# Kernel tuning notes

Hardware: AMD Instinct MI355X
Metric: run time of the kernel (lower is better)

The kernel has to match this reference:

```python
import jax, jax.numpy as jnp
import numpy as np
from jax import lax

N = 4096
IN_DIM, HID, OUT_DIM = 8, 64, 4
N_CONV = 10


def setup_inputs() -> dict:
    key = jax.random.key(0)
    ks = jax.random.split(key, 16)
    s = 0.05
    inp = {
        "inputs": jax.random.normal(ks[0], (N, IN_DIM), jnp.float32),
        "emb_w": jax.random.normal(ks[1], (IN_DIM, HID), jnp.float32) * s,
        "emb_b": jnp.zeros((HID,), jnp.float32),
        "q_w": jax.random.normal(ks[2], (HID, HID), jnp.float32) * s,
        "q_b": jnp.zeros((HID,), jnp.float32),
        "k_w": jax.random.normal(ks[3], (HID, HID), jnp.float32) * s,
        "k_b": jnp.zeros((HID,), jnp.float32),
        # 10 asymmetric conv layers: 1x3 kernel, 3x1 kernel, PReLU scalar (torch default 0.25)
        "conv_w1": jax.random.normal(ks[4], (N_CONV, 3), jnp.float32) * 0.3,
        "conv_w2": jax.random.normal(ks[5], (N_CONV, 3), jnp.float32) * 0.3,
        "conv_a": jnp.full((N_CONV,), 0.25, jnp.float32),
        "gcn_w": jax.random.normal(ks[6], (OUT_DIM, HID), jnp.float32) * s,
        "gcn_b": jnp.zeros((HID,), jnp.float32),
        "gcn_a": jnp.float32(0.25),
        "mlp_w1": jax.random.normal(ks[7], (HID, HID // 2), jnp.float32) * s,
        "mlp_b1": jnp.zeros((HID // 2,), jnp.float32),
        "mlp_w2": jax.random.normal(ks[8], (HID // 2, OUT_DIM), jnp.float32) * s,
        "mlp_b2": jnp.zeros((OUT_DIM,), jnp.float32),
    }
    return inp


def _asym_layer(x, w1, w2, a):
    # x: [1,1,N,N]; w1 -> 1x3 conv, w2 -> 3x1 conv, a -> PReLU scalar
    k1 = w1.reshape(1, 1, 1, 3)
    k2 = w2.reshape(1, 1, 3, 1)
    dn = ("NCHW", "OIHW", "NCHW")
    o = (lax.conv_general_dilated(x, k1, (1, 1), [(0, 0), (1, 1)], dimension_numbers=dn)
         + lax.conv_general_dilated(x, k2, (1, 1), [(1, 1), (0, 0)], dimension_numbers=dn))
    return jnp.where(o >= 0, o, a * o)


def reference(inputs, emb_w, emb_b, q_w, q_b, k_w, k_b,
              conv_w1, conv_w2, conv_a,
              gcn_w, gcn_b, gcn_a, mlp_w1, mlp_b1, mlp_w2, mlp_b2):
    o = inputs[:, 4:]                                   # [N, 4]
    x = inputs @ emb_w + emb_b                          # [N, H]
    q = x @ q_w + q_b                                   # [N, D]
    k = x @ k_w + k_b                                   # [N, D]
    scores = (q @ k.T) / jnp.sqrt(jnp.float32(k.shape[-1]))
    attn = jax.nn.softmax(scores, axis=-1)              # [N, N]

    h = attn[None, None]                                # [1,1,N,N]
    for i in range(N_CONV):
        h = _asym_layer(h, conv_w1[i], conv_w2[i], conv_a[i])
    conv_features = h[0, 0]                             # [N, N]

    mask = (jax.nn.sigmoid(conv_features) > 0.5).astype(attn.dtype)
    adjacency = mask * attn                             # [N, N]
    calc = adjacency @ o                                # [N, 4]

    g = calc @ gcn_w + gcn_b
    g = jnp.where(g >= 0, g, gcn_a * g)                 # PReLU
    m = jnp.maximum(g @ mlp_w1 + mlp_b1, 0.0)
    return m @ mlp_w2 + mlp_b2                          # [N, 4]
```

## Files before the change

kernel.cpp:

```cpp
#include <hip/hip_runtime.h>
#include <hip/hip_fp16.h>

#define NROWS 4096
#define HID 64

typedef _Float16 f16x8 __attribute__((ext_vector_type(8)));
typedef float f32x4 __attribute__((ext_vector_type(4)));

static __device__ __forceinline__ __half2 u2h(unsigned u) {
  __half2 h; __builtin_memcpy(&h, &u, 4); return h;
}
static __device__ __forceinline__ unsigned h2u(__half2 h) {
  unsigned u; __builtin_memcpy(&u, &h, 4); return u;
}

__global__ __launch_bounds__(256) void k_embed(
    const float* __restrict__ inp, const float* __restrict__ emb_w,
    const float* __restrict__ emb_b, const float* __restrict__ q_w,
    const float* __restrict__ q_b, const float* __restrict__ k_w,
    const float* __restrict__ k_b, __half* __restrict__ qh,
    __half* __restrict__ kh, float* __restrict__ opk) {
  int t = threadIdx.x;
  int rr = t >> 6;
  int c = t & 63;
  int row = blockIdx.x * 4 + rr;
  __shared__ float in_s[4][8];
  __shared__ float x_s[4][64];
  if (c < 8) in_s[rr][c] = inp[row * 8 + c];
  __syncthreads();
  float acc = emb_b[c];
#pragma unroll
  for (int i = 0; i < 8; ++i) acc += in_s[rr][i] * emb_w[i * 64 + c];
  x_s[rr][c] = acc;
  __syncthreads();
  float qa = q_b[c], ka = k_b[c];
#pragma unroll
  for (int i = 0; i < 64; ++i) {
    float xv = x_s[rr][i];
    qa += xv * q_w[i * 64 + c];
    ka += xv * k_w[i * 64 + c];
  }
  qh[row * 64 + c] = __float2half(qa * 0.125f);
  kh[row * 64 + c] = __float2half(ka);
  if (c < 4) opk[row * 4 + c] = inp[row * 8 + 4 + c];
}

__global__ __launch_bounds__(512, 2) void k_scores(
    const __half* __restrict__ qh, const __half* __restrict__ kh,
    float* __restrict__ S) {
  __shared__ float redm[8][16];
  __shared__ float reds[8][16];
  int t = threadIdx.x;
  int w = t >> 6;
  int l = t & 63;
  int m16 = l & 15;
  int g4 = l >> 4;
  int rb = blockIdx.x * 16;
  const uint4* qq = (const uint4*)qh;
  const uint4* kk = (const uint4*)kh;
  int qrow = rb + m16;
  f16x8 a0 = __builtin_bit_cast(f16x8, qq[qrow * 8 + g4]);
  f16x8 a1 = __builtin_bit_cast(f16x8, qq[qrow * 8 + 4 + g4]);
  f32x4 acc[32];
#pragma unroll
  for (int i = 0; i < 32; ++i) acc[i] = (f32x4){0.f, 0.f, 0.f, 0.f};
#pragma unroll
  for (int i = 0; i < 32; ++i) {
    int kcol = (w * 32 + i) * 16 + m16;
    f16x8 b0 = __builtin_bit_cast(f16x8, kk[kcol * 8 + g4]);
    f16x8 b1 = __builtin_bit_cast(f16x8, kk[kcol * 8 + 4 + g4]);
    acc[i] = __builtin_amdgcn_mfma_f32_16x16x32_f16(a0, b0, acc[i], 0, 0, 0);
    acc[i] = __builtin_amdgcn_mfma_f32_16x16x32_f16(a1, b1, acc[i], 0, 0, 0);
  }
  float m4[4] = {-1e30f, -1e30f, -1e30f, -1e30f};
#pragma unroll
  for (int i = 0; i < 32; ++i) {
#pragma unroll
    for (int c = 0; c < 4; ++c) m4[c] = fmaxf(m4[c], acc[i][c]);
  }
#pragma unroll
  for (int off = 1; off < 16; off <<= 1) {
#pragma unroll
    for (int c = 0; c < 4; ++c) m4[c] = fmaxf(m4[c], __shfl_xor(m4[c], off, 64));
  }
  if (m16 == 0) {
#pragma unroll
    for (int c = 0; c < 4; ++c) redm[w][g4 * 4 + c] = m4[c];
  }
  __syncthreads();
#pragma unroll
  for (int c = 0; c < 4; ++c) {
    float mm = redm[0][g4 * 4 + c];
#pragma unroll
    for (int ww = 1; ww < 8; ++ww) mm = fmaxf(mm, redm[ww][g4 * 4 + c]);
    m4[c] = mm;
  }
  float s4[4] = {0.f, 0.f, 0.f, 0.f};
#pragma unroll
  for (int i = 0; i < 32; ++i) {
#pragma unroll
    for (int c = 0; c < 4; ++c) {
      float e = __expf(acc[i][c] - m4[c]);
      acc[i][c] = e;
      s4[c] += e;
    }
  }
#pragma unroll
  for (int off = 1; off < 16; off <<= 1) {
#pragma unroll
    for (int c = 0; c < 4; ++c) s4[c] += __shfl_xor(s4[c], off, 64);
  }
  if (m16 == 0) {
#pragma unroll
    for (int c = 0; c < 4; ++c) reds[w][g4 * 4 + c] = s4[c];
  }
  __syncthreads();
  float li[4];
#pragma unroll
  for (int c = 0; c < 4; ++c) {
    float ss = reds[0][g4 * 4 + c];
#pragma unroll
    for (int ww = 1; ww < 8; ++ww) ss += reds[ww][g4 * 4 + c];
    li[c] = 1.0f / ss;
  }
#pragma unroll
  for (int i = 0; i < 32; ++i) {
    int col = (w * 32 + i) * 16 + m16;
#pragma unroll
    for (int c = 0; c < 4; ++c) {
      S[(size_t)(rb + g4 * 4 + c) * NROWS + col] = acc[i][c] * li[c];
    }
  }
}

#define C5D 130
#define C5H 74
#define C5OW 236
#define C5OH 54
#define C5GX 18
#define C5GY 76

__global__ __launch_bounds__(512, 2) void k_conv5(
    const float* __restrict__ attn, float* __restrict__ partial,
    const float* __restrict__ w1p, const float* __restrict__ w2p,
    const float* __restrict__ ap, const float* __restrict__ opk) {
  __shared__ unsigned buf[C5H * C5D];
  int tid = threadIdx.x;
  int bx = blockIdx.x, by = blockIdx.y;
  int gi0 = by * C5OH - 10;
  int gj0 = bx * C5OW - 10;
  bool edge = (bx == 0) || (bx == C5GX - 1) || (by == 0) || (by == C5GY - 1);
  if (!edge) {
    for (int idx = tid; idx < C5H * 128; idx += 512) {
      int r = idx >> 7, d = idx & 127;
      float2 v = *(const float2*)(attn + (size_t)(gi0 + r) * NROWS + gj0 + 2 * d);
      buf[r * C5D + d] =
          h2u(__float22half2_rn(make_float2(v.x * 256.f, v.y * 256.f)));
    }
  } else {
    for (int idx = tid; idx < C5H * 128; idx += 512) {
      int r = idx >> 7, d = idx & 127;
      int gi = gi0 + r, gj = gj0 + 2 * d;
      float a = 0.f, b = 0.f;
      if ((unsigned)gi < (unsigned)NROWS) {
        if ((unsigned)gj < (unsigned)NROWS) a = attn[(size_t)gi * NROWS + gj] * 256.f;
        if ((unsigned)(gj + 1) < (unsigned)NROWS) b = attn[(size_t)gi * NROWS + gj + 1] * 256.f;
      }
      buf[r * C5D + d] = h2u(__float22half2_rn(make_float2(a, b)));
    }
  }
  __syncthreads();

  int wv = tid >> 6, l = tid & 63;
  int rb = 1 + 9 * wv;
  int doff = 2 * l;
  __half2 CM0 = __float2half2_rn(1.f), CM1 = __float2half2_rn(1.f);
  if (edge) {
    float m0 = ((unsigned)(gj0 + 4 * l + 0) < (unsigned)NROWS) ? 1.f : 0.f;
    float m1 = ((unsigned)(gj0 + 4 * l + 1) < (unsigned)NROWS) ? 1.f : 0.f;
    float m2 = ((unsigned)(gj0 + 4 * l + 2) < (unsigned)NROWS) ? 1.f : 0.f;
    float m3 = ((unsigned)(gj0 + 4 * l + 3) < (unsigned)NROWS) ? 1.f : 0.f;
    CM0 = __float22half2_rn(make_float2(m0, m1));
    CM1 = __float22half2_rn(make_float2(m2, m3));
  }

  for (int p = 0; p < 10; ++p) {
    __half2 W10 = __float2half2_rn(w1p[3 * p]);
    __half2 W12 = __float2half2_rn(w1p[3 * p + 2]);
    __half2 WC  = __float2half2_rn(w1p[3 * p + 1] + w2p[3 * p + 1]);
    __half2 W20 = __float2half2_rn(w2p[3 * p]);
    __half2 W22 = __float2half2_rn(w2p[3 * p + 2]);
    __half2 AL  = __float2half2_rn(ap[p]);
    uint2 Vm = *(uint2*)&buf[(rb - 1) * C5D + doff];
    uint2 Vc = *(uint2*)&buf[rb * C5D + doff];
    uint2 dfirst, dlast;
#pragma unroll
    for (int s = 0; s < 9; ++s) {
      int r = rb + s;
      uint2 Vp = *(uint2*)&buf[(r + 1) * C5D + doff];
      unsigned Lm1 = (unsigned)__builtin_amdgcn_update_dpp(
          0, (int)Vc.y, 0x138, 0xF, 0xF, true);
      unsigned Hp1 = (unsigned)__builtin_amdgcn_update_dpp(
          0, (int)Vc.x, 0x130, 0xF, 0xF, true);
      unsigned SL0 = __builtin_amdgcn_alignbit(Vc.x, Lm1, 16);
      unsigned SR0 = __builtin_amdgcn_alignbit(Vc.y, Vc.x, 16);
      unsigned SR1 = __builtin_amdgcn_alignbit(Hp1, Vc.y, 16);
      __half2 o0 = __hmul2(WC, u2h(Vc.x));
      o0 = __hfma2(W10, u2h(SL0), o0);
      o0 = __hfma2(W12, u2h(SR0), o0);
      o0 = __hfma2(W20, u2h(Vm.x), o0);
      o0 = __hfma2(W22, u2h(Vp.x), o0);
      __half2 o1 = __hmul2(WC, u2h(Vc.y));
      o1 = __hfma2(W10, u2h(SR0), o1);
      o1 = __hfma2(W12, u2h(SR1), o1);
      o1 = __hfma2(W20, u2h(Vm.y), o1);
      o1 = __hfma2(W22, u2h(Vp.y), o1);
      {
        unsigned u0 = h2u(o0), ua0 = h2u(__hmul2(AL, o0)), r0;
        asm("v_pk_max_f16 %0, %1, %2" : "=v"(r0) : "v"(u0), "v"(ua0));
        o0 = u2h(r0);
        unsigned u1 = h2u(o1), ua1 = h2u(__hmul2(AL, o1)), r1;
        asm("v_pk_max_f16 %0, %1, %2" : "=v"(r1) : "v"(u1), "v"(ua1));
        o1 = u2h(r1);
      }
      if (edge) {
        o0 = __hmul2(o0, CM0);
        o1 = __hmul2(o1, CM1);
        if ((unsigned)(gi0 + r) >= (unsigned)NROWS) {
          o0 = __float2half2_rn(0.f);
          o1 = __float2half2_rn(0.f);
        }
      }
      uint2 res = {h2u(o0), h2u(o1)};
      if (s == 0) dfirst = res;
      else if (s == 8) dlast = res;
      else *(uint2*)&buf[r * C5D + doff] = res;
      Vm = Vc; Vc = Vp;
    }
    __syncthreads();
    *(uint2*)&buf[rb * C5D + doff] = dfirst;
    *(uint2*)&buf[(rb + 8) * C5D + doff] = dlast;
    __syncthreads();
  }

  const unsigned* fin = buf;
  int i = tid >> 3;
  int part = tid & 7;
  int gi = gi0 + 10 + i;
  float a0 = 0.f, a1 = 0.f, a2 = 0.f, a3 = 0.f;
  if (i < C5OH && gi < NROWS) {
    const float4* op = (const float4*)opk;
    for (int g = part; g < 59; g += 8) {
      int jc = 10 + 4 * g;
      int gj = gj0 + jc;
      if (gj + 3 < NROWS) {
        unsigned d0 = fin[(10 + i) * C5D + (jc >> 1)];
        unsigned d1 = fin[(10 + i) * C5D + (jc >> 1) + 1];
        __half2 h0 = u2h(d0), h1 = u2h(d1);
        float4 av = *(const float4*)(attn + (size_t)gi * NROWS + gj);
        if (__low2float(h0) > 0.f)  { float4 o = op[gj + 0]; a0 += av.x * o.x; a1 += av.x * o.y; a2 += av.x * o.z; a3 += av.x * o.w; }
        if (__high2float(h0) > 0.f) { float4 o = op[gj + 1]; a0 += av.y * o.x; a1 += av.y * o.y; a2 += av.y * o.z; a3 += av.y * o.w; }
        if (__low2float(h1) > 0.f)  { float4 o = op[gj + 2]; a0 += av.z * o.x; a1 += av.z * o.y; a2 += av.z * o.z; a3 += av.z * o.w; }
        if (__high2float(h1) > 0.f) { float4 o = op[gj + 3]; a0 += av.w * o.x; a1 += av.w * o.y; a2 += av.w * o.z; a3 += av.w * o.w; }
      }
    }
  }
#pragma unroll
  for (int off = 1; off < 8; off <<= 1) {
    a0 += __shfl_xor(a0, off, 64);
    a1 += __shfl_xor(a1, off, 64);
    a2 += __shfl_xor(a2, off, 64);
    a3 += __shfl_xor(a3, off, 64);
  }
  if (part == 0 && i < C5OH && gi < NROWS) {
    float4 r = {a0, a1, a2, a3};
    *(float4*)&partial[((size_t)bx * NROWS + gi) * 4] = r;
  }
}

__global__ __launch_bounds__(64) void k_head(
    const float* __restrict__ partial, const float* __restrict__ gcn_w,
    const float* __restrict__ gcn_b, const float* __restrict__ gcn_a,
    const float* __restrict__ w1, const float* __restrict__ b1,
    const float* __restrict__ w2, const float* __restrict__ b2,
    float* __restrict__ out) {
  int row = blockIdx.x;
  int t = threadIdx.x;
  __shared__ float c4[4];
  __shared__ float gs[64];
  __shared__ float ms[32];
  {
    int c = t & 3, gg = t >> 2;
    float s = partial[((size_t)gg * NROWS + row) * 4 + c];
    if (gg < C5GX - 16)
      s += partial[((size_t)(gg + 16) * NROWS + row) * 4 + c];
#pragma unroll
    for (int off = 4; off < 64; off <<= 1) s += __shfl_xor(s, off, 64);
    if (t < 4) c4[t] = s;
  }
  __syncthreads();
  float g = gcn_b[t];
#pragma unroll
  for (int d = 0; d < 4; ++d) g += c4[d] * gcn_w[d * 64 + t];
  float ga = gcn_a[0];
  gs[t] = (g >= 0.f) ? g : ga * g;
  __syncthreads();
  if (t < 32) {
    float mm = b1[t];
#pragma unroll
    for (int i = 0; i < 64; ++i) mm += gs[i] * w1[i * 32 + t];
    ms[t] = fmaxf(mm, 0.f);
  }
  __syncthreads();
  if (t < 4) {
    float o = b2[t];
#pragma unroll
    for (int i = 0; i < 32; ++i) o += ms[i] * w2[i * 4 + t];
    out[row * 4 + t] = o;
  }
}

extern "C" void kernel_launch(void* const* d_in, const int* in_sizes, int n_in,
                              void* d_out, int out_size, void* d_ws, size_t ws_size,
                              hipStream_t stream) {
  (void)in_sizes; (void)n_in; (void)out_size; (void)ws_size;
  const float* inp    = (const float*)d_in[0];
  const float* emb_w  = (const float*)d_in[1];
  const float* emb_b  = (const float*)d_in[2];
  const float* q_w    = (const float*)d_in[3];
  const float* q_b    = (const float*)d_in[4];
  const float* k_w    = (const float*)d_in[5];
  const float* k_b    = (const float*)d_in[6];
  const float* conv_w1 = (const float*)d_in[7];
  const float* conv_w2 = (const float*)d_in[8];
  const float* conv_a  = (const float*)d_in[9];
  const float* gcn_w  = (const float*)d_in[10];
  const float* gcn_b  = (const float*)d_in[11];
  const float* gcn_a  = (const float*)d_in[12];
  const float* mlp_w1 = (const float*)d_in[13];
  const float* mlp_b1 = (const float*)d_in[14];
  const float* mlp_w2 = (const float*)d_in[15];
  const float* mlp_b2 = (const float*)d_in[16];
  float* out = (float*)d_out;

  const size_t NN = (size_t)NROWS * NROWS;
  float* A       = (float*)d_ws;
  float* partial = A + NN;
  float* qhf     = partial + (size_t)18 * NROWS * 4;
  float* khf     = qhf + (size_t)NROWS * HID / 2;
  float* opk     = khf + (size_t)NROWS * HID / 2;

  k_embed<<<NROWS / 4, 256, 0, stream>>>(inp, emb_w, emb_b, q_w, q_b, k_w, k_b,
                                         (__half*)qhf, (__half*)khf, opk);
  k_scores<<<NROWS / 16, 512, 0, stream>>>((const __half*)qhf,
                                           (const __half*)khf, A);
  k_conv5<<<dim3(C5GX, C5GY), 512, 0, stream>>>(A, partial, conv_w1, conv_w2,
                                                conv_a, opk);
  k_head<<<NROWS, 64, 0, stream>>>(partial, gcn_w, gcn_b, gcn_a, mlp_w1, mlp_b1,
                                   mlp_w2, mlp_b2, out);
}
```

Baseline: 121.2 us.

## Store attention matrix in fp16 pre-scaled, resize conv tiles, batch head rows

The scores kernel now writes the softmax output as fp16 pre-multiplied by 256 instead of fp32, halving the N×N write and the conv kernel's read traffic. The conv kernel loads the half2 data straight into shared memory without conversion, and the final mask-times-attn accumulation reads fp16 attn and rescales by 1/256 at the end. Conv tile height drops from 54 to 46 output rows (8 rows per wave), which raises halo overhead but may improve occupancy via smaller shared memory. The head kernel processes 8 rows per 512-thread block instead of one row per 64-thread block. Using fp16 attn values in the adjacency product adds rounding error.

```diff
diff --git a/kernel.cpp b/kernel.cpp
--- a/kernel.cpp
+++ b/kernel.cpp
@@ -47,7 +47,7 @@
 
 __global__ __launch_bounds__(512, 2) void k_scores(
     const __half* __restrict__ qh, const __half* __restrict__ kh,
-    float* __restrict__ S) {
+    __half* __restrict__ Sh) {
   __shared__ float redm[8][16];
   __shared__ float reds[8][16];
   int t = threadIdx.x;
@@ -121,58 +121,59 @@
     float ss = reds[0][g4 * 4 + c];
 #pragma unroll
     for (int ww = 1; ww < 8; ++ww) ss += reds[ww][g4 * 4 + c];
-    li[c] = 1.0f / ss;
+    li[c] = 256.0f / ss;
   }
 #pragma unroll
   for (int i = 0; i < 32; ++i) {
     int col = (w * 32 + i) * 16 + m16;
 #pragma unroll
     for (int c = 0; c < 4; ++c) {
-      S[(size_t)(rb + g4 * 4 + c) * NROWS + col] = acc[i][c] * li[c];
+      Sh[(size_t)(rb + g4 * 4 + c) * NROWS + col] = __float2half(acc[i][c] * li[c]);
     }
   }
 }
 
 #define C5D 130
-#define C5H 74
+#define C5H 66
 #define C5OW 236
-#define C5OH 54
+#define C5OH 46
 #define C5GX 18
-#define C5GY 76
+#define C5GY 90
 
 __global__ __launch_bounds__(512, 2) void k_conv5(
-    const float* __restrict__ attn, float* __restrict__ partial,
+    const __half* __restrict__ attnh, float* __restrict__ partial,
     const float* __restrict__ w1p, const float* __restrict__ w2p,
     const float* __restrict__ ap, const float* __restrict__ opk) {
   __shared__ unsigned buf[C5H * C5D];
+  const unsigned* Shd = (const unsigned*)attnh;
   int tid = threadIdx.x;
   int bx = blockIdx.x, by = blockIdx.y;
   int gi0 = by * C5OH - 10;
   int gj0 = bx * C5OW - 10;
   bool edge = (bx == 0) || (bx == C5GX - 1) || (by == 0) || (by == C5GY - 1);
   if (!edge) {
+    int dbase = gj0 >> 1;
     for (int idx = tid; idx < C5H * 128; idx += 512) {
       int r = idx >> 7, d = idx & 127;
-      float2 v = *(const float2*)(attn + (size_t)(gi0 + r) * NROWS + gj0 + 2 * d);
-      buf[r * C5D + d] =
-          h2u(__float22half2_rn(make_float2(v.x * 256.f, v.y * 256.f)));
+      buf[r * C5D + d] = Shd[(size_t)(gi0 + r) * (NROWS / 2) + dbase + d];
     }
   } else {
     for (int idx = tid; idx < C5H * 128; idx += 512) {
       int r = idx >> 7, d = idx & 127;
       int gi = gi0 + r, gj = gj0 + 2 * d;
-      float a = 0.f, b = 0.f;
+      __half a = __float2half(0.f), b = a;
       if ((unsigned)gi < (unsigned)NROWS) {
-        if ((unsigned)gj < (unsigned)NROWS) a = attn[(size_t)gi * NROWS + gj] * 256.f;
-        if ((unsigned)(gj + 1) < (unsigned)NROWS) b = attn[(size_t)gi * NROWS + gj + 1] * 256.f;
+        if ((unsigned)gj < (unsigned)NROWS) a = attnh[(size_t)gi * NROWS + gj];
+        if ((unsigned)(gj + 1) < (unsigned)NROWS) b = attnh[(size_t)gi * NROWS + gj + 1];
       }
-      buf[r * C5D + d] = h2u(__float22half2_rn(make_float2(a, b)));
+      __half2 p; p.x = a; p.y = b;
+      buf[r * C5D + d] = h2u(p);
     }
   }
   __syncthreads();
 
   int wv = tid >> 6, l = tid & 63;
-  int rb = 1 + 9 * wv;
+  int rb = 1 + 8 * wv;
   int doff = 2 * l;
   __half2 CM0 = __float2half2_rn(1.f), CM1 = __float2half2_rn(1.f);
   if (edge) {
@@ -195,7 +196,7 @@
     uint2 Vc = *(uint2*)&buf[rb * C5D + doff];
     uint2 dfirst, dlast;
 #pragma unroll
-    for (int s = 0; s < 9; ++s) {
+    for (int s = 0; s < 8; ++s) {
       int r = rb + s;
       uint2 Vp = *(uint2*)&buf[(r + 1) * C5D + doff];
       unsigned Lm1 = (unsigned)__builtin_amdgcn_update_dpp(
@@ -233,13 +234,13 @@
       }
       uint2 res = {h2u(o0), h2u(o1)};
       if (s == 0) dfirst = res;
-      else if (s == 8) dlast = res;
+      else if (s == 7) dlast = res;
       else *(uint2*)&buf[r * C5D + doff] = res;
       Vm = Vc; Vc = Vp;
     }
     __syncthreads();
     *(uint2*)&buf[rb * C5D + doff] = dfirst;
-    *(uint2*)&buf[(rb + 8) * C5D + doff] = dlast;
+    *(uint2*)&buf[(rb + 7) * C5D + doff] = dlast;
     __syncthreads();
   }
 
@@ -257,11 +258,13 @@
         unsigned d0 = fin[(10 + i) * C5D + (jc >> 1)];
         unsigned d1 = fin[(10 + i) * C5D + (jc >> 1) + 1];
         __half2 h0 = u2h(d0), h1 = u2h(d1);
-        float4 av = *(const float4*)(attn + (size_t)gi * NROWS + gj);
-        if (__low2float(h0) > 0.f)  { float4 o = op[gj + 0]; a0 += av.x * o.x; a1 += av.x * o.y; a2 += av.x * o.z; a3 += av.x * o.w; }
-        if (__high2float(h0) > 0.f) { float4 o = op[gj + 1]; a0 += av.y * o.x; a1 += av.y * o.y; a2 += av.y * o.z; a3 += av.y * o.w; }
-        if (__low2float(h1) > 0.f)  { float4 o = op[gj + 2]; a0 += av.z * o.x; a1 += av.z * o.y; a2 += av.z * o.z; a3 += av.z * o.w; }
-        if (__high2float(h1) > 0.f) { float4 o = op[gj + 3]; a0 += av.w * o.x; a1 += av.w * o.y; a2 += av.w * o.z; a3 += av.w * o.w; }
+        unsigned a01 = Shd[(size_t)gi * (NROWS / 2) + (gj >> 1)];
+        unsigned a23 = Shd[(size_t)gi * (NROWS / 2) + (gj >> 1) + 1];
+        __half2 av01 = u2h(a01), av23 = u2h(a23);
+        if (__low2float(h0) > 0.f)  { float av = __low2float(av01);  float4 o = op[gj + 0]; a0 += av * o.x; a1 += av * o.y; a2 += av * o.z; a3 += av * o.w; }
+        if (__high2float(h0) > 0.f) { float av = __high2float(av01); float4 o = op[gj + 1]; a0 += av * o.x; a1 += av * o.y; a2 += av * o.z; a3 += av * o.w; }
+        if (__low2float(h1) > 0.f)  { float av = __low2float(av23);  float4 o = op[gj + 2]; a0 += av * o.x; a1 += av * o.y; a2 += av * o.z; a3 += av * o.w; }
+        if (__high2float(h1) > 0.f) { float av = __high2float(av23); float4 o = op[gj + 3]; a0 += av * o.x; a1 += av * o.y; a2 += av * o.z; a3 += av * o.w; }
       }
     }
   }
@@ -273,50 +276,53 @@
     a3 += __shfl_xor(a3, off, 64);
   }
   if (part == 0 && i < C5OH && gi < NROWS) {
-    float4 r = {a0, a1, a2, a3};
+    const float s = 1.0f / 256.0f;
+    float4 r = {a0 * s, a1 * s, a2 * s, a3 * s};
     *(float4*)&partial[((size_t)bx * NROWS + gi) * 4] = r;
   }
 }
 
-__global__ __launch_bounds__(64) void k_head(
+__global__ __launch_bounds__(512) void k_head(
     const float* __restrict__ partial, const float* __restrict__ gcn_w,
     const float* __restrict__ gcn_b, const float* __restrict__ gcn_a,
     const float* __restrict__ w1, const float* __restrict__ b1,
     const float* __restrict__ w2, const float* __restrict__ b2,
     float* __restrict__ out) {
-  int row = blockIdx.x;
   int t = threadIdx.x;
-  __shared__ float c4[4];
-  __shared__ float gs[64];
-  __shared__ float ms[32];
+  int rw = t >> 6;
+  int tl = t & 63;
+  int row = blockIdx.x * 8 + rw;
+  __shared__ float c4[8][4];
+  __shared__ float gs[8][64];
+  __shared__ float ms[8][32];
   {
-    int c = t & 3, gg = t >> 2;
+    int c = tl & 3, gg = tl >> 2;
     float s = partial[((size_t)gg * NROWS + row) * 4 + c];
     if (gg < C5GX - 16)
       s += partial[((size_t)(gg + 16) * NROWS + row) * 4 + c];
 #pragma unroll
     for (int off = 4; off < 64; off <<= 1) s += __shfl_xor(s, off, 64);
-    if (t < 4) c4[t] = s;
-  }
-  __syncthreads();
-  float g = gcn_b[t];
-#pragma unroll
-  for (int d = 0; d < 4; ++d) g += c4[d] * gcn_w[d * 64 + t];
+    if (tl < 4) c4[rw][tl] = s;
+  }
+  __syncthreads();
+  float g = gcn_b[tl];
+#pragma unroll
+  for (int d = 0; d < 4; ++d) g += c4[rw][d] * gcn_w[d * 64 + tl];
   float ga = gcn_a[0];
-  gs[t] = (g >= 0.f) ? g : ga * g;
-  __syncthreads();
-  if (t < 32) {
-    float mm = b1[t];
-#pragma unroll
-    for (int i = 0; i < 64; ++i) mm += gs[i] * w1[i * 32 + t];
-    ms[t] = fmaxf(mm, 0.f);
-  }
-  __syncthreads();
-  if (t < 4) {
-    float o = b2[t];
-#pragma unroll
-    for (int i = 0; i < 32; ++i) o += ms[i] * w2[i * 4 + t];
-    out[row * 4 + t] = o;
+  gs[rw][tl] = (g >= 0.f) ? g : ga * g;
+  __syncthreads();
+  if (tl < 32) {
+    float mm = b1[tl];
+#pragma unroll
+    for (int i = 0; i < 64; ++i) mm += gs[rw][i] * w1[i * 32 + tl];
+    ms[rw][tl] = fmaxf(mm, 0.f);
+  }
+  __syncthreads();
+  if (tl < 4) {
+    float o = b2[tl];
+#pragma unroll
+    for (int i = 0; i < 32; ++i) o += ms[rw][i] * w2[i * 4 + tl];
+    out[row * 4 + tl] = o;
   }
 }
 
@@ -344,8 +350,8 @@
   float* out = (float*)d_out;
 
   const size_t NN = (size_t)NROWS * NROWS;
-  float* A       = (float*)d_ws;
-  float* partial = A + NN;
+  float* Sh      = (float*)d_ws;
+  float* partial = Sh + NN / 2;
   float* qhf     = partial + (size_t)18 * NROWS * 4;
   float* khf     = qhf + (size_t)NROWS * HID / 2;
   float* opk     = khf + (size_t)NROWS * HID / 2;
@@ -353,9 +359,9 @@
   k_embed<<<NROWS / 4, 256, 0, stream>>>(inp, emb_w, emb_b, q_w, q_b, k_w, k_b,
                                          (__half*)qhf, (__half*)khf, opk);
   k_scores<<<NROWS / 16, 512, 0, stream>>>((const __half*)qhf,
-                                           (const __half*)khf, A);
-  k_conv5<<<dim3(C5GX, C5GY), 512, 0, stream>>>(A, partial, conv_w1, conv_w2,
-                                                conv_a, opk);
-  k_head<<<NROWS, 64, 0, stream>>>(partial, gcn_w, gcn_b, gcn_a, mlp_w1, mlp_b1,
-                                   mlp_w2, mlp_b2, out);
-}
+                                           (const __half*)khf, (__half*)Sh);
+  k_conv5<<<dim3(C5GX, C5GY), 512, 0, stream>>>((const __half*)Sh, partial,
+                                                conv_w1, conv_w2, conv_a, opk);
+  k_head<<<NROWS / 8, 512, 0, stream>>>(partial, gcn_w, gcn_b, gcn_a, mlp_w1,
+                                        mlp_b1, mlp_w2, mlp_b2, out);
+}
```

Result: faster. 110.1 us (median of 2 runs) (-9.2%).
